# Kernel optimization log

Hardware: AMD Instinct MI355X
Metric: run time of the kernel (lower is better)

The kernel has to match this reference:

```python
import jax, jax.numpy as jnp
import numpy as np

EMBED_DIM = 512
NUM_HEADS = 8
NUM_LAYERS = 2
LN_EPS = 1e-5


def setup_inputs() -> dict:
    key = jax.random.key(0)
    ks = jax.random.split(key, 12)
    B, S, E, L = 8, 1024, EMBED_DIM, NUM_LAYERS
    scale = 1.0 / np.sqrt(E)  # kaiming-ish init scale for 1x1 conv weights
    return {
        "x": jax.random.normal(ks[0], (B, S, E), jnp.float32),
        "adj": jax.random.uniform(ks[1], (S, S), jnp.float32),
        "Wq": jax.random.normal(ks[2], (L, E, E), jnp.float32) * scale,
        "bq": jnp.zeros((L, E), jnp.float32),
        "Wk": jax.random.normal(ks[3], (L, E, E), jnp.float32) * scale,
        "bk": jnp.zeros((L, E), jnp.float32),
        "Wv": jax.random.normal(ks[4], (L, E, E), jnp.float32) * scale,
        "bv": jnp.zeros((L, E), jnp.float32),
        "Wo": jax.random.normal(ks[5], (L, E, E), jnp.float32) * scale,
        "bo": jnp.zeros((L, E), jnp.float32),
        "gamma": jnp.ones((L, E), jnp.float32),
        "beta": jnp.zeros((L, E), jnp.float32),
    }


def _layer_norm(x, g, b):
    mu = jnp.mean(x, axis=-1, keepdims=True)
    var = jnp.mean(jnp.square(x - mu), axis=-1, keepdims=True)
    return (x - mu) * jax.lax.rsqrt(var + LN_EPS) * g + b


def reference(x, adj, Wq, bq, Wk, bk, Wv, bv, Wo, bo, gamma, beta):
    B, S, E = x.shape
    H = NUM_HEADS
    D = E // H
    inv_sqrt_d = 1.0 / np.sqrt(D)
    for l in range(Wq.shape[0]):
        # 1x1 Conv2d over channel dim == per-token linear: out_f = sum_e W[f,e] x_e + b_f
        q = (jnp.einsum('bse,fe->bsf', x, Wq[l]) + bq[l]).reshape(B, S, H, D).transpose(0, 2, 1, 3)
        k = (jnp.einsum('bse,fe->bsf', x, Wk[l]) + bk[l]).reshape(B, S, H, D).transpose(0, 2, 1, 3)
        v = (jnp.einsum('bse,fe->bsf', x, Wv[l]) + bv[l]).reshape(B, S, H, D).transpose(0, 2, 1, 3)
        # adjacency-gated scaled dot-product attention: multiplicative mask BEFORE softmax
        scores = jnp.einsum('bhqd,bhkd->bhqk', q, k) * inv_sqrt_d
        scores = scores * adj  # broadcast [S,S] over [B,H,S,S]
        attn = jax.nn.softmax(scores, axis=-1)
        out = jnp.einsum('bhqk,bhkd->bhqd', attn, v)
        out = out.transpose(0, 2, 1, 3).reshape(B, S, E)
        out = jnp.einsum('bse,fe->bsf', out, Wo[l]) + bo[l]
        x = _layer_norm(x + out, gamma[l], beta[l])
    return x
```

## Files before the change

### kernel.cpp

```cpp
#include <hip/hip_runtime.h>
#include <stdint.h>

typedef _Float16 f16;
typedef _Float16 f16x8 __attribute__((ext_vector_type(8)));
typedef _Float16 f16x4 __attribute__((ext_vector_type(4)));
typedef float f32x4 __attribute__((ext_vector_type(4)));

constexpr int EMB = 512;
constexpr int SEQ = 1024;
constexpr int NH = 8;
constexpr int DHEAD = 64;
constexpr int NTOK = 8192;

#define GAS __attribute__((address_space(1)))
#define LAS __attribute__((address_space(3)))

#if __has_builtin(__builtin_amdgcn_exp2f)
#define EXP2F(x) __builtin_amdgcn_exp2f(x)
#else
#define EXP2F(x) exp2f(x)
#endif

static __device__ __forceinline__ void gload_lds16(const void* g, void* l) {
  __builtin_amdgcn_global_load_lds((const GAS void*)g, (LAS void*)l, 16, 0, 0);
}


__global__ __launch_bounds__(256) void k_prep(const float* __restrict__ x, const float* __restrict__ adj,
                                              const float* __restrict__ Wq, const float* __restrict__ Wk,
                                              const float* __restrict__ Wv, const float* __restrict__ Wo,
                                              const float* __restrict__ bq, const float* __restrict__ bk,
                                              const float* __restrict__ bv,
                                              f16* __restrict__ xh, f16* __restrict__ wqkv,
                                              f16* __restrict__ wo, f16* __restrict__ adjP,
                                              float* __restrict__ bqkv) {
  const int bid = blockIdx.x;
  if (bid < 2048) {
    int i = (bid * 256 + threadIdx.x) * 8;
    float4 a = *(const float4*)(x + i);
    float4 b = *(const float4*)(x + i + 4);
    f16x8 h = {(f16)a.x, (f16)a.y, (f16)a.z, (f16)a.w, (f16)b.x, (f16)b.y, (f16)b.z, (f16)b.w};
    *(f16x8*)(xh + i) = h;
  } else if (bid < 3584) {
    int tid = (bid - 2048) * 256 + threadIdx.x;
    if (tid < 2 * 1536 * 128) {
      int e4 = tid & 127;
      int f = (tid >> 7) % 1536;
      int l = tid / (128 * 1536);
      int part = f >> 9, fr = f & 511;
      const float* src = (part == 0 ? Wq : part == 1 ? Wk : Wv) + (size_t)l * EMB * EMB + (size_t)fr * EMB + e4 * 4;
      float4 v = *(const float4*)src;
      f16x4 hv = {(f16)v.x, (f16)v.y, (f16)v.z, (f16)v.w};
      *(f16x4*)(wqkv + ((size_t)l * 1536 + f) * EMB + e4 * 4) = hv;
    }
    if (tid < 2 * 512 * 128) {
      int e4 = tid & 127;
      int f = (tid >> 7) % 512;
      int l = tid / (128 * 512);
      float4 v = *(const float4*)(Wo + (size_t)l * EMB * EMB + (size_t)f * EMB + e4 * 4);
      f16x4 hv = {(f16)v.x, (f16)v.y, (f16)v.z, (f16)v.w};
      *(f16x4*)(wo + ((size_t)l * 512 + f) * EMB + e4 * 4) = hv;
    }
  } else if (bid < 4608) {
    int tid = (bid - 3584) * 256 + threadIdx.x;
    int lo = tid & 15, t = (tid >> 4) & 15, qrow = tid >> 8;
    const float c = 0.125f * 1.44269504088896f;
    const float* row = adj + (size_t)qrow * SEQ + t * 64 + lo;
    f16x4 v = {(f16)(row[0] * c), (f16)(row[16] * c), (f16)(row[32] * c), (f16)(row[48] * c)};
    *(f16x4*)(adjP + (size_t)tid * 4) = v;
  } else {
    int tid = (bid - 4608) * 256 + threadIdx.x;
    if (tid < 2 * 1536) {
      int f = tid % 1536, l = tid / 1536;
      int part = f >> 9, fr = f & 511;
      bqkv[tid] = (part == 0 ? bq : part == 1 ? bk : bv)[l * EMB + fr];
    }
  }
}


template <int MODE>
__global__ __launch_bounds__(512) void k_gemm(const f16* __restrict__ A, const f16* __restrict__ Bw,
                                              const float* __restrict__ bias, f16* __restrict__ Uout,
                                              f16* __restrict__ Qo, f16* __restrict__ Ko,
                                              f16* __restrict__ Vt) {
  __shared__ f16x8 sA[2][1024];
  __shared__ f16x8 sB[2][1024];
  const int tid = threadIdx.x;
  const int lane = tid & 63;
  const int lanelow = lane & 15, lanehi = lane >> 4;
  const int wave = tid >> 6;
  const int wm = wave >> 1;
  const int wn = wave & 1;
  const int flat = blockIdx.x;
  const int mt = (flat & 7) * 8 + ((flat >> 3) & 7);
  const int nt = flat >> 6;
  const int m0 = mt * 128, n0 = nt * 128;

  f32x4 acc[2][4] = {};

  const f16* aB = A + (size_t)m0 * EMB;
  const f16* bB = Bw + (size_t)n0 * EMB;

  int srow[2], scl[2];
#pragma unroll
  for (int p = 0; p < 2; ++p) {
    int c = p * 512 + tid;
    srow[p] = c >> 3;
    scl[p] = (c & 7) ^ (srow[p] & 7);
  }

#define GSTAGE(ktv, bufv)                                                                     \
  {                                                                                           \
    _Pragma("unroll") for (int p = 0; p < 2; ++p) {                                           \
      int c = p * 512 + tid;                                                                  \
      gload_lds16(aB + (size_t)srow[p] * EMB + (ktv) + scl[p] * 8, (char*)sA[bufv] + c * 16); \
      gload_lds16(bB + (size_t)srow[p] * EMB + (ktv) + scl[p] * 8, (char*)sB[bufv] + c * 16); \
    }                                                                                         \
  }

  GSTAGE(0, 0);
  __syncthreads();

  int cur = 0;
  for (int t = 0; t < 8; ++t) {
    if (t < 7) GSTAGE((t + 1) * 64, cur ^ 1);
#pragma unroll
    for (int ks = 0; ks < 2; ++ks) {
      f16x8 af[2], bf[4];
#pragma unroll
      for (int m = 0; m < 2; ++m) {
        int r = wm * 32 + m * 16 + lanelow;
        af[m] = sA[cur][r * 8 + ((ks * 4 + lanehi) ^ (r & 7))];
      }
#pragma unroll
      for (int n = 0; n < 4; ++n) {
        int r = wn * 64 + n * 16 + lanelow;
        bf[n] = sB[cur][r * 8 + ((ks * 4 + lanehi) ^ (r & 7))];
      }
      __builtin_amdgcn_s_setprio(1);
#pragma unroll
      for (int m = 0; m < 2; ++m)
#pragma unroll
        for (int n = 0; n < 4; ++n)
          acc[m][n] = __builtin_amdgcn_mfma_f32_16x16x32_f16(af[m], bf[n], acc[m][n], 0, 0, 0);
      __builtin_amdgcn_s_setprio(0);
    }
    __syncthreads();
    cur ^= 1;
  }
#undef GSTAGE

#pragma unroll
  for (int n = 0; n < 4; ++n) {
    int col = n0 + wn * 64 + n * 16 + lanelow;
    float bv = bias[col];
    if (MODE == 1 && (col >> 9) == 2) {
      int fr = col & 511, hh = fr >> 6, d = fr & 63;
#pragma unroll
      for (int m = 0; m < 2; ++m) {
        int rbase = m0 + wm * 32 + m * 16 + lanehi * 4;
        int b = rbase >> 10, s = rbase & 1023;
        f16x4 pv = {(f16)(acc[m][n][0] + bv), (f16)(acc[m][n][1] + bv),
                    (f16)(acc[m][n][2] + bv), (f16)(acc[m][n][3] + bv)};
        *(f16x4*)(Vt + ((size_t)(b * NH + hh) * DHEAD + d) * SEQ + s) = pv;
      }
    } else {
#pragma unroll
      for (int m = 0; m < 2; ++m) {
        int rbase = m0 + wm * 32 + m * 16 + lanehi * 4;
#pragma unroll
        for (int j = 0; j < 4; ++j) {
          float v = acc[m][n][j] + bv;
          int row = rbase + j;
          if (MODE == 0) {
            Uout[(size_t)row * EMB + col] = (f16)v;
          } else {
            int part = col >> 9, fr = col & 511;
            int hh = fr >> 6, d = fr & 63;
            int b = row >> 10, s = row & 1023;
            int bh = b * NH + hh;
            if (part == 0)
              Qo[((size_t)bh * SEQ + s) * DHEAD + d] = (f16)v;
            else
              Ko[((size_t)bh * SEQ + s) * DHEAD + d] = (f16)v;
          }
        }
      }
    }
  }
}


__global__ __launch_bounds__(512) void k_attn(const f16* __restrict__ Q, const f16* __restrict__ K,
                                              const f16* __restrict__ Vt, const f16* __restrict__ adjP,
                                              f16* __restrict__ Ob) {
  __shared__ __align__(16) f16 sK[2][8192];
  __shared__ __align__(16) f16 sV[2][8192];
  __shared__ __align__(16) f16 Pl[8 * 1024];
  const int tid = threadIdx.x;
  const int lane = tid & 63;
  const int lanelow = lane & 15, lanehi = lane >> 4;
  const int wave = tid >> 6;
  f16* Plw = Pl + wave * 1024;

  const int flat = blockIdx.x;
  const int bh = (flat & 7) * 8 + ((flat >> 3) & 7);
  const int qblk = flat >> 6;
  const int b = bh >> 3, hh = bh & 7;
  const int q0 = qblk * 128 + wave * 16;

  const f16* Kbase = K + (size_t)bh * SEQ * DHEAD;
  const f16* Vbase = Vt + (size_t)bh * DHEAD * SEQ;

  int kr[2], kc[2], vr[2], vc[2];
#pragma unroll
  for (int p = 0; p < 2; ++p) {
    int c = p * 512 + tid;
    kr[p] = c >> 3;
    kc[p] = (c & 7) ^ (kr[p] & 7);
    vr[p] = c >> 4;
    vc[p] = (c & 15) ^ (vr[p] & 7);
  }

#define STAGE(tv, bufv)                                                                         \
  {                                                                                             \
    const int kts = (tv)*128;                                                                   \
    _Pragma("unroll") for (int p = 0; p < 2; ++p) {                                             \
      int c = p * 512 + tid;                                                                    \
      gload_lds16(Kbase + (size_t)(kts + kr[p]) * DHEAD + kc[p] * 8, (char*)sK[bufv] + c * 16); \
      gload_lds16(Vbase + (size_t)vr[p] * SEQ + kts + vc[p] * 8, (char*)sV[bufv] + c * 16);     \
    }                                                                                           \
  }

  f16x8 qf[2];
#pragma unroll
  for (int ks = 0; ks < 2; ++ks)
    qf[ks] = *(const f16x8*)(Q + ((size_t)bh * SEQ + q0 + lanelow) * DHEAD + ks * 32 + lanehi * 8);

  const f16* Ab = adjP + ((size_t)(q0 + lanehi * 4) * 256 + lanelow) * 4;
  f16x4 ab[4];
#define LOAD_A(tv)                                                           \
  {                                                                          \
    _Pragma("unroll") for (int j = 0; j < 4; ++j)                            \
        ab[j] = *(const f16x4*)(Ab + ((size_t)j * 256 + (tv)*16) * 4);       \
  }

  f32x4 oacc[4] = {};
  float lpart[4] = {};

  STAGE(0, 0);
  LOAD_A(0);
  __syncthreads();

  int cur = 0;
  for (int t = 0; t < 8; ++t) {
    if (t < 7) STAGE(t + 1, cur ^ 1);

    const f16* sKc = sK[cur];
    const f16* sVc = sV[cur];

#pragma unroll
    for (int hs = 0; hs < 2; ++hs) {
      const int t2 = t * 2 + hs;

      f32x4 sacc[4] = {};
#pragma unroll
      for (int ks = 0; ks < 2; ++ks) {
        f16x8 kf[4];
#pragma unroll
        for (int n = 0; n < 4; ++n) {
          int r = hs * 64 + n * 16 + lanelow;
          kf[n] = *(const f16x8*)(sKc + (r * 8 + ((ks * 4 + lanehi) ^ (r & 7))) * 8);
        }
        __builtin_amdgcn_s_setprio(1);
#pragma unroll
        for (int n = 0; n < 4; ++n)
          sacc[n] = __builtin_amdgcn_mfma_f32_16x16x32_f16(qf[ks], kf[n], sacc[n], 0, 0, 0);
        __builtin_amdgcn_s_setprio(0);
      }

      f16x4 acur[4];
#pragma unroll
      for (int j = 0; j < 4; ++j) acur[j] = ab[j];
      if (t2 < 15) LOAD_A(t2 + 1);

#pragma unroll
      for (int nh = 0; nh < 2; ++nh) {
#pragma unroll
        for (int j = 0; j < 4; ++j) {
          const int prow = lanehi * 4 + j;
          const f16x4 a4 = acur[j];
#pragma unroll
          for (int nn = 0; nn < 2; ++nn) {
            const int n = nh * 2 + nn;
            float p = EXP2F(sacc[n][j] * (float)a4[n]);
            lpart[j] += p;
            Plw[prow * 64 + (((n * 2 + (lanelow >> 3)) ^ (prow & 7)) * 8) + (lanelow & 7)] = (f16)p;
          }
        }
        f16x8 pa, vf[4];
        pa = *(const f16x8*)(Plw + lanelow * 64 + (((nh * 4 + lanehi) ^ (lanelow & 7)) * 8));
#pragma unroll
        for (int n = 0; n < 4; ++n) {
          int r = n * 16 + lanelow;
          vf[n] = *(const f16x8*)(sVc + (r * 16 + ((hs * 8 + nh * 4 + lanehi) ^ (r & 7))) * 8);
        }
        __builtin_amdgcn_s_setprio(1);
#pragma unroll
        for (int n = 0; n < 4; ++n)
          oacc[n] = __builtin_amdgcn_mfma_f32_16x16x32_f16(pa, vf[n], oacc[n], 0, 0, 0);
        __builtin_amdgcn_s_setprio(0);
      }
    }

    __syncthreads();
    cur ^= 1;
  }
#undef STAGE
#undef LOAD_A

  float linv[4];
#pragma unroll
  for (int j = 0; j < 4; ++j) {
    float l = lpart[j];
#pragma unroll
    for (int off = 1; off < 16; off <<= 1) l += __shfl_xor(l, off, 16);
    linv[j] = 1.0f / l;
  }
#pragma unroll
  for (int n = 0; n < 4; ++n)
#pragma unroll
    for (int j = 0; j < 4; ++j) {
      int qrow = q0 + lanehi * 4 + j;
      float v = oacc[n][j] * linv[j];
      Ob[((size_t)b * SEQ + qrow) * EMB + hh * DHEAD + n * 16 + lanelow] = (f16)v;
    }
}


template <int INH>
__global__ __launch_bounds__(256) void k_ln(const float* __restrict__ xf, const f16* __restrict__ xh_in,
                                            const f16* __restrict__ Uin,
                                            const float* __restrict__ gamma, const float* __restrict__ beta,
                                            float* __restrict__ xout, f16* __restrict__ xh_out) {
  const int row = blockIdx.x * 4 + (threadIdx.x >> 6);
  const int lane = threadIdx.x & 63;
  const size_t base = (size_t)row * EMB + lane * 8;
  float u[8];
  {
    f16x8 uh = *(const f16x8*)(Uin + base);
    if (INH) {
      f16x8 xh8 = *(const f16x8*)(xh_in + base);
#pragma unroll
      for (int i = 0; i < 8; ++i) u[i] = (float)xh8[i] + (float)uh[i];
    } else {
      float4 a0 = *(const float4*)(xf + base);
      float4 a1 = *(const float4*)(xf + base + 4);
      u[0] = a0.x + (float)uh[0]; u[1] = a0.y + (float)uh[1];
      u[2] = a0.z + (float)uh[2]; u[3] = a0.w + (float)uh[3];
      u[4] = a1.x + (float)uh[4]; u[5] = a1.y + (float)uh[5];
      u[6] = a1.z + (float)uh[6]; u[7] = a1.w + (float)uh[7];
    }
  }
  float s = 0.f;
#pragma unroll
  for (int i = 0; i < 8; ++i) s += u[i];
#pragma unroll
  for (int off = 1; off < 64; off <<= 1) s += __shfl_xor(s, off, 64);
  const float mu = s * (1.0f / EMB);
  float v = 0.f;
#pragma unroll
  for (int i = 0; i < 8; ++i) { float d = u[i] - mu; v += d * d; }
#pragma unroll
  for (int off = 1; off < 64; off <<= 1) v += __shfl_xor(v, off, 64);
  const float rs = rsqrtf(v * (1.0f / EMB) + 1e-5f);
  const int ci = lane * 8;
  float4 g0 = *(const float4*)(gamma + ci);
  float4 g1 = *(const float4*)(gamma + ci + 4);
  float4 b0 = *(const float4*)(beta + ci);
  float4 b1 = *(const float4*)(beta + ci + 4);
  float g[8] = {g0.x, g0.y, g0.z, g0.w, g1.x, g1.y, g1.z, g1.w};
  float be[8] = {b0.x, b0.y, b0.z, b0.w, b1.x, b1.y, b1.z, b1.w};
  float o[8];
#pragma unroll
  for (int i = 0; i < 8; ++i) o[i] = (u[i] - mu) * rs * g[i] + be[i];
  if (xout) {
    float4 o0 = {o[0], o[1], o[2], o[3]}, o1 = {o[4], o[5], o[6], o[7]};
    *(float4*)(xout + base) = o0;
    *(float4*)(xout + base + 4) = o1;
  }
  if (xh_out) {
    f16x8 hv = {(f16)o[0], (f16)o[1], (f16)o[2], (f16)o[3], (f16)o[4], (f16)o[5], (f16)o[6], (f16)o[7]};
    *(f16x8*)(xh_out + base) = hv;
  }
}


extern "C" void kernel_launch(void* const* d_in, const int* in_sizes, int n_in,
                              void* d_out, int out_size, void* d_ws, size_t ws_size,
                              hipStream_t stream) {
  (void)in_sizes; (void)n_in; (void)out_size; (void)ws_size;
  const float* x = (const float*)d_in[0];
  const float* adj = (const float*)d_in[1];
  const float* Wq = (const float*)d_in[2];
  const float* bq = (const float*)d_in[3];
  const float* Wk = (const float*)d_in[4];
  const float* bk = (const float*)d_in[5];
  const float* Wv = (const float*)d_in[6];
  const float* bv = (const float*)d_in[7];
  const float* Wo = (const float*)d_in[8];
  const float* bo = (const float*)d_in[9];
  const float* gamma = (const float*)d_in[10];
  const float* beta = (const float*)d_in[11];

  char* ws = (char*)d_ws;
  size_t off = 0;
  auto alloc = [&](size_t bytes) {
    char* p = ws + off;
    off += (bytes + 255) & ~(size_t)255;
    return p;
  };
  f16* wqkv = (f16*)alloc((size_t)2 * 1536 * 512 * sizeof(f16));
  f16* wo = (f16*)alloc((size_t)2 * 512 * 512 * sizeof(f16));
  float* bqkv = (float*)alloc((size_t)2 * 1536 * sizeof(float));
  f16* adjP = (f16*)alloc((size_t)SEQ * SEQ * sizeof(f16));
  f16* xh = (f16*)alloc((size_t)NTOK * EMB * sizeof(f16));
  f16* Qb = (f16*)alloc((size_t)NTOK * EMB * sizeof(f16));
  f16* Kb = (f16*)alloc((size_t)NTOK * EMB * sizeof(f16));
  f16* Vtb = (f16*)alloc((size_t)NTOK * EMB * sizeof(f16));
  f16* Ob = (f16*)alloc((size_t)NTOK * EMB * sizeof(f16));
  f16* U = (f16*)alloc((size_t)NTOK * EMB * sizeof(f16));

  k_prep<<<4620, 256, 0, stream>>>(x, adj, Wq, Wk, Wv, Wo, bq, bk, bv,
                                   xh, wqkv, wo, adjP, bqkv);

  for (int l = 0; l < 2; ++l) {
    k_gemm<1><<<768, 512, 0, stream>>>(xh, wqkv + (size_t)l * 1536 * 512, bqkv + l * 1536,
                                       nullptr, Qb, Kb, Vtb);
    k_attn<<<512, 512, 0, stream>>>(Qb, Kb, Vtb, adjP, Ob);
    k_gemm<0><<<256, 512, 0, stream>>>(Ob, wo + (size_t)l * 512 * 512, bo + l * 512,
                                       U, nullptr, nullptr, nullptr);
    if (l == 0)
      k_ln<0><<<2048, 256, 0, stream>>>(x, nullptr, U, gamma, beta, nullptr, xh);
    else
      k_ln<1><<<2048, 256, 0, stream>>>(nullptr, xh, U, gamma + 512, beta + 512, (float*)d_out, nullptr);
  }
}
```

Measured before the change: 157.4 us.

## Fuse output projection GEMM with residual add and LayerNorm

Replaces the separate O-projection GEMM and LayerNorm kernels with one kernel. Each block computes 32 full rows of 512 columns, so the row statistics are reduced in-kernel through LDS. This removes the intermediate U buffer round-trip and one launch per layer. The cost is that every block streams the whole 512x512 weight matrix, which means large LDS use and low occupancy. The variance now uses the one-pass E[x²]−mu² form, which is less numerically robust.

After: 158.1 us. No clear change (+0.5%).

```diff
diff --git a/kernel.cpp b/kernel.cpp
--- a/kernel.cpp
+++ b/kernel.cpp
@@ -79,11 +79,10 @@
 }
 
 
-template <int MODE>
-__global__ __launch_bounds__(512) void k_gemm(const f16* __restrict__ A, const f16* __restrict__ Bw,
-                                              const float* __restrict__ bias, f16* __restrict__ Uout,
-                                              f16* __restrict__ Qo, f16* __restrict__ Ko,
-                                              f16* __restrict__ Vt) {
+__global__ __launch_bounds__(512) void k_gemmqkv(const f16* __restrict__ A, const f16* __restrict__ Bw,
+                                                 const float* __restrict__ bias,
+                                                 f16* __restrict__ Qo, f16* __restrict__ Ko,
+                                                 f16* __restrict__ Vt) {
   __shared__ f16x8 sA[2][1024];
   __shared__ f16x8 sB[2][1024];
   const int tid = threadIdx.x;
@@ -155,7 +154,7 @@
   for (int n = 0; n < 4; ++n) {
     int col = n0 + wn * 64 + n * 16 + lanelow;
     float bv = bias[col];
-    if (MODE == 1 && (col >> 9) == 2) {
+    if ((col >> 9) == 2) {
       int fr = col & 511, hh = fr >> 6, d = fr & 63;
 #pragma unroll
       for (int m = 0; m < 2; ++m) {
@@ -173,18 +172,14 @@
         for (int j = 0; j < 4; ++j) {
           float v = acc[m][n][j] + bv;
           int row = rbase + j;
-          if (MODE == 0) {
-            Uout[(size_t)row * EMB + col] = (f16)v;
-          } else {
-            int part = col >> 9, fr = col & 511;
-            int hh = fr >> 6, d = fr & 63;
-            int b = row >> 10, s = row & 1023;
-            int bh = b * NH + hh;
-            if (part == 0)
-              Qo[((size_t)bh * SEQ + s) * DHEAD + d] = (f16)v;
-            else
-              Ko[((size_t)bh * SEQ + s) * DHEAD + d] = (f16)v;
-          }
+          int part = col >> 9, fr = col & 511;
+          int hh = fr >> 6, d = fr & 63;
+          int b = row >> 10, s = row & 1023;
+          int bh = b * NH + hh;
+          if (part == 0)
+            Qo[((size_t)bh * SEQ + s) * DHEAD + d] = (f16)v;
+          else
+            Ko[((size_t)bh * SEQ + s) * DHEAD + d] = (f16)v;
         }
       }
     }
@@ -340,60 +335,139 @@
 
 
 template <int INH>
-__global__ __launch_bounds__(256) void k_ln(const float* __restrict__ xf, const f16* __restrict__ xh_in,
-                                            const f16* __restrict__ Uin,
-                                            const float* __restrict__ gamma, const float* __restrict__ beta,
-                                            float* __restrict__ xout, f16* __restrict__ xh_out) {
-  const int row = blockIdx.x * 4 + (threadIdx.x >> 6);
-  const int lane = threadIdx.x & 63;
-  const size_t base = (size_t)row * EMB + lane * 8;
-  float u[8];
-  {
-    f16x8 uh = *(const f16x8*)(Uin + base);
-    if (INH) {
-      f16x8 xh8 = *(const f16x8*)(xh_in + base);
-#pragma unroll
-      for (int i = 0; i < 8; ++i) u[i] = (float)xh8[i] + (float)uh[i];
-    } else {
-      float4 a0 = *(const float4*)(xf + base);
-      float4 a1 = *(const float4*)(xf + base + 4);
-      u[0] = a0.x + (float)uh[0]; u[1] = a0.y + (float)uh[1];
-      u[2] = a0.z + (float)uh[2]; u[3] = a0.w + (float)uh[3];
-      u[4] = a1.x + (float)uh[4]; u[5] = a1.y + (float)uh[5];
-      u[6] = a1.z + (float)uh[6]; u[7] = a1.w + (float)uh[7];
-    }
-  }
-  float s = 0.f;
-#pragma unroll
-  for (int i = 0; i < 8; ++i) s += u[i];
-#pragma unroll
-  for (int off = 1; off < 64; off <<= 1) s += __shfl_xor(s, off, 64);
-  const float mu = s * (1.0f / EMB);
-  float v = 0.f;
-#pragma unroll
-  for (int i = 0; i < 8; ++i) { float d = u[i] - mu; v += d * d; }
-#pragma unroll
-  for (int off = 1; off < 64; off <<= 1) v += __shfl_xor(v, off, 64);
-  const float rs = rsqrtf(v * (1.0f / EMB) + 1e-5f);
-  const int ci = lane * 8;
-  float4 g0 = *(const float4*)(gamma + ci);
-  float4 g1 = *(const float4*)(gamma + ci + 4);
-  float4 b0 = *(const float4*)(beta + ci);
-  float4 b1 = *(const float4*)(beta + ci + 4);
-  float g[8] = {g0.x, g0.y, g0.z, g0.w, g1.x, g1.y, g1.z, g1.w};
-  float be[8] = {b0.x, b0.y, b0.z, b0.w, b1.x, b1.y, b1.z, b1.w};
-  float o[8];
-#pragma unroll
-  for (int i = 0; i < 8; ++i) o[i] = (u[i] - mu) * rs * g[i] + be[i];
-  if (xout) {
-    float4 o0 = {o[0], o[1], o[2], o[3]}, o1 = {o[4], o[5], o[6], o[7]};
-    *(float4*)(xout + base) = o0;
-    *(float4*)(xout + base + 4) = o1;
-  }
-  if (xh_out) {
-    f16x8 hv = {(f16)o[0], (f16)o[1], (f16)o[2], (f16)o[3], (f16)o[4], (f16)o[5], (f16)o[6], (f16)o[7]};
-    *(f16x8*)(xh_out + base) = hv;
-  }
+__global__ __launch_bounds__(512) void k_oprojln(const f16* __restrict__ A, const f16* __restrict__ Bw,
+                                                 const float* __restrict__ bias,
+                                                 const float* __restrict__ resf, const f16* __restrict__ resh,
+                                                 const float* __restrict__ gamma, const float* __restrict__ beta,
+                                                 f16* __restrict__ xh_out, float* __restrict__ fout) {
+  __shared__ f16x8 sA[2][256];
+  __shared__ f16x8 sB[2][4096];
+  const int tid = threadIdx.x;
+  const int lane = tid & 63;
+  const int lanelow = lane & 15, lanehi = lane >> 4;
+  const int wave = tid >> 6;
+  const int m0 = blockIdx.x * 32;
+
+  f32x4 acc[2][4] = {};
+
+  const f16* aB = A + (size_t)m0 * EMB;
+
+  const int arow = tid >> 3, ach = (tid & 7) ^ (arow & 7);
+  int brow[8], bch[8];
+#pragma unroll
+  for (int p = 0; p < 8; ++p) {
+    int c = p * 512 + tid;
+    brow[p] = c >> 3;
+    bch[p] = (c & 7) ^ (brow[p] & 7);
+  }
+
+#define GSTAGE(ktv, bufv)                                                                        \
+  {                                                                                              \
+    if (tid < 256)                                                                               \
+      gload_lds16(aB + (size_t)arow * EMB + (ktv) + ach * 8, (char*)sA[bufv] + tid * 16);        \
+    _Pragma("unroll") for (int p = 0; p < 8; ++p) {                                              \
+      int c = p * 512 + tid;                                                                     \
+      gload_lds16(Bw + (size_t)brow[p] * EMB + (ktv) + bch[p] * 8, (char*)sB[bufv] + c * 16);    \
+    }                                                                                            \
+  }
+
+  GSTAGE(0, 0);
+  __syncthreads();
+
+  int cur = 0;
+  for (int t = 0; t < 8; ++t) {
+    if (t < 7) GSTAGE((t + 1) * 64, cur ^ 1);
+#pragma unroll
+    for (int ks = 0; ks < 2; ++ks) {
+      f16x8 af[2], bf[4];
+#pragma unroll
+      for (int m = 0; m < 2; ++m) {
+        int r = m * 16 + lanelow;
+        af[m] = sA[cur][r * 8 + ((ks * 4 + lanehi) ^ (r & 7))];
+      }
+#pragma unroll
+      for (int n = 0; n < 4; ++n) {
+        int r = wave * 64 + n * 16 + lanelow;
+        bf[n] = sB[cur][r * 8 + ((ks * 4 + lanehi) ^ (r & 7))];
+      }
+      __builtin_amdgcn_s_setprio(1);
+#pragma unroll
+      for (int m = 0; m < 2; ++m)
+#pragma unroll
+        for (int n = 0; n < 4; ++n)
+          acc[m][n] = __builtin_amdgcn_mfma_f32_16x16x32_f16(af[m], bf[n], acc[m][n], 0, 0, 0);
+      __builtin_amdgcn_s_setprio(0);
+    }
+    __syncthreads();
+    cur ^= 1;
+  }
+#undef GSTAGE
+
+  float* sS1 = (float*)sA;
+  float* sS2 = (float*)sA + 256;
+
+  float bv[4], g4[4], b4[4];
+#pragma unroll
+  for (int n = 0; n < 4; ++n) {
+    int col = wave * 64 + n * 16 + lanelow;
+    bv[n] = bias[col];
+    g4[n] = gamma[col];
+    b4[n] = beta[col];
+  }
+
+#pragma unroll
+  for (int m = 0; m < 2; ++m)
+#pragma unroll
+    for (int j = 0; j < 4; ++j) {
+      const int row32 = m * 16 + lanehi * 4 + j;
+      const size_t row = m0 + row32;
+      float s1 = 0.f, s2 = 0.f;
+#pragma unroll
+      for (int n = 0; n < 4; ++n) {
+        const int col = wave * 64 + n * 16 + lanelow;
+        float r = INH ? (float)resh[row * EMB + col] : resf[row * EMB + col];
+        float u = acc[m][n][j] + bv[n] + r;
+        acc[m][n][j] = u;
+        s1 += u;
+        s2 += u * u;
+      }
+#pragma unroll
+      for (int off = 1; off < 16; off <<= 1) {
+        s1 += __shfl_xor(s1, off, 16);
+        s2 += __shfl_xor(s2, off, 16);
+      }
+      if (lanelow == 0) {
+        sS1[wave * 32 + row32] = s1;
+        sS2[wave * 32 + row32] = s2;
+      }
+    }
+  __syncthreads();
+
+#pragma unroll
+  for (int m = 0; m < 2; ++m)
+#pragma unroll
+    for (int j = 0; j < 4; ++j) {
+      const int row32 = m * 16 + lanehi * 4 + j;
+      const size_t row = m0 + row32;
+      float S1 = 0.f, S2 = 0.f;
+#pragma unroll
+      for (int w = 0; w < 8; ++w) {
+        S1 += sS1[w * 32 + row32];
+        S2 += sS2[w * 32 + row32];
+      }
+      const float mu = S1 * (1.0f / EMB);
+      const float var = S2 * (1.0f / EMB) - mu * mu;
+      const float rs = rsqrtf(var + 1e-5f);
+#pragma unroll
+      for (int n = 0; n < 4; ++n) {
+        const int col = wave * 64 + n * 16 + lanelow;
+        float o = (acc[m][n][j] - mu) * rs * g4[n] + b4[n];
+        if (INH)
+          fout[row * EMB + col] = o;
+        else
+          xh_out[row * EMB + col] = (f16)o;
+      }
+    }
 }
 
 
@@ -430,20 +504,18 @@
   f16* Kb = (f16*)alloc((size_t)NTOK * EMB * sizeof(f16));
   f16* Vtb = (f16*)alloc((size_t)NTOK * EMB * sizeof(f16));
   f16* Ob = (f16*)alloc((size_t)NTOK * EMB * sizeof(f16));
-  f16* U = (f16*)alloc((size_t)NTOK * EMB * sizeof(f16));
 
   k_prep<<<4620, 256, 0, stream>>>(x, adj, Wq, Wk, Wv, Wo, bq, bk, bv,
                                    xh, wqkv, wo, adjP, bqkv);
 
   for (int l = 0; l < 2; ++l) {
-    k_gemm<1><<<768, 512, 0, stream>>>(xh, wqkv + (size_t)l * 1536 * 512, bqkv + l * 1536,
-                                       nullptr, Qb, Kb, Vtb);
+    k_gemmqkv<<<768, 512, 0, stream>>>(xh, wqkv + (size_t)l * 1536 * 512, bqkv + l * 1536,
+                                       Qb, Kb, Vtb);
     k_attn<<<512, 512, 0, stream>>>(Qb, Kb, Vtb, adjP, Ob);
-    k_gemm<0><<<256, 512, 0, stream>>>(Ob, wo + (size_t)l * 512 * 512, bo + l * 512,
-                                       U, nullptr, nullptr, nullptr);
     if (l == 0)
-      k_ln<0><<<2048, 256, 0, stream>>>(x, nullptr, U, gamma, beta, nullptr, xh);
+      k_oprojln<0><<<256, 512, 0, stream>>>(Ob, wo, bo, x, nullptr, gamma, beta, xh, nullptr);
     else
-      k_ln<1><<<2048, 256, 0, stream>>>(nullptr, xh, U, gamma + 512, beta + 512, (float*)d_out, nullptr);
+      k_oprojln<1><<<256, 512, 0, stream>>>(Ob, wo + (size_t)512 * 512, bo + 512, nullptr, xh,
+                                            gamma + 512, beta + 512, nullptr, (float*)d_out);
   }
 }
```
